# Kernel optimization log

Measured on AMD Instinct MI355X. Metric: run time of the kernel, lower is better.

## Reference

```python
import jax, jax.numpy as jnp
import numpy as np

B, D, K, H = 8192, 1024, 4096, 8


def setup_inputs() -> dict:
    key = jax.random.key(0)
    k1, k2 = jax.random.split(key)
    inputs = jax.random.normal(k1, (B, 1, D), dtype=jnp.float32)
    # Per-head codebooks; original init decays scale by init_decay_weight**hix,
    # emulate with a 0.5**h decay so later heads model smaller residuals.
    decay = (0.5 ** jnp.arange(H, dtype=jnp.float32)).reshape(H, 1, 1)
    codebooks = jax.random.normal(k2, (H, K, D), dtype=jnp.float32) * decay
    return {"inputs": inputs, "codebooks": codebooks}


def reference(inputs, codebooks):
    """Hierarchical refinement quantizer, eval path (hard argmin selection).

    Cascade over heads: distances to codebook -> argmin -> gather embedding
    -> subtract from residual -> next head. Returns (quantized_sum, codes).
    """
    x = inputs[:, 0, :]                      # [B, D]
    resid = x
    quantized = jnp.zeros_like(x)
    codes = []
    n_heads = codebooks.shape[0]
    for h in range(n_heads):                 # fixed, small head count
        E = codebooks[h]                     # [K, D]
        # squared euclidean distances: ||r||^2 - 2 r.E^T + ||E||^2  -> [B, K]
        dist = (
            jnp.sum(resid * resid, axis=-1, keepdims=True)
            - 2.0 * jnp.einsum("bd,kd->bk", resid, E)
            + jnp.sum(E * E, axis=-1)
        )
        idx = jnp.argmin(dist, axis=-1)      # [B]
        onehot = jax.nn.one_hot(idx, E.shape[0], dtype=resid.dtype)  # [B, K]
        q = onehot @ E                       # [B, D] gathered embedding
        quantized = quantized + q
        resid = resid - q
        codes.append(idx)
    vq_codes = jnp.stack(codes, axis=1)      # [B, H]
    return quantized, vq_codes
```

## Files before the change

kernel.cpp:

```cpp
#include <hip/hip_runtime.h>

#define B_ 8192
#define D_ 1024
#define K_ 4096
#define H_ 8

#define BM 128
#define BN 128
#define BK 32
#define NBLK 64
#define NCAND 6

typedef __attribute__((ext_vector_type(8))) short short8v;
typedef __attribute__((ext_vector_type(4))) float f32x4;

#define FINF 3.4e38f
#define IBIG 0x7fffffff

__device__ __forceinline__ void amin(float& v, int& i, float v2, int i2) {
    if (v2 < v || (v2 == v && i2 < i)) { v = v2; i = i2; }
}

__device__ __forceinline__ unsigned short f2bf_rn(float x) {
    unsigned int u = __float_as_uint(x);
    unsigned int r = (u + 0x7fffu + ((u >> 16) & 1u)) >> 16;
    return (unsigned short)r;
}

__device__ __forceinline__ void gload16(const unsigned short* g, unsigned short* l) {
    __builtin_amdgcn_global_load_lds(
        (const __attribute__((address_space(1))) void*)g,
        (__attribute__((address_space(3))) void*)l, 16, 0, 0);
}

__global__ __launch_bounds__(256) void cbconv_kernel(const float* __restrict__ E,
                                                     unsigned short* __restrict__ hi,
                                                     float* __restrict__ eeh) {
    const int row = blockIdx.x;
    const int t = threadIdx.x;
    float4 v = reinterpret_cast<const float4*>(E + (size_t)row * D_)[t];
    ushort4 h;
    h.x = f2bf_rn(v.x); h.y = f2bf_rn(v.y);
    h.z = f2bf_rn(v.z); h.w = f2bf_rn(v.w);
    reinterpret_cast<ushort4*>(hi + (size_t)row * D_)[t] = h;
    float s = v.x * v.x + v.y * v.y + v.z * v.z + v.w * v.w;
    #pragma unroll
    for (int m = 1; m < 64; m <<= 1) s += __shfl_xor(s, m);
    __shared__ float ls[4];
    if ((t & 63) == 0) ls[t >> 6] = s;
    __syncthreads();
    if (t == 0) eeh[row] = (ls[0] + ls[1]) + (ls[2] + ls[3]);
}

__global__ __launch_bounds__(256) void init_kernel(const float* __restrict__ x,
                                                   float* __restrict__ resid,
                                                   float* __restrict__ rr,
                                                   unsigned short* __restrict__ rhi) {
    const int b = blockIdx.x;
    const int t = threadIdx.x;
    float4 v = reinterpret_cast<const float4*>(x + (size_t)b * D_)[t];
    reinterpret_cast<float4*>(resid + (size_t)b * D_)[t] = v;
    ushort4 h;
    h.x = f2bf_rn(v.x); h.y = f2bf_rn(v.y);
    h.z = f2bf_rn(v.z); h.w = f2bf_rn(v.w);
    reinterpret_cast<ushort4*>(rhi + (size_t)b * D_)[t] = h;
    float s = v.x * v.x + v.y * v.y + v.z * v.z + v.w * v.w;
    #pragma unroll
    for (int m = 1; m < 64; m <<= 1) s += __shfl_xor(s, m);
    __shared__ float ls[4];
    if ((t & 63) == 0) ls[t >> 6] = s;
    __syncthreads();
    if (t == 0) rr[b] = (ls[0] + ls[1]) + (ls[2] + ls[3]);
}

__global__ __launch_bounds__(256) void score_mfma_kernel(
    const unsigned short* __restrict__ Ch,
    const unsigned short* __restrict__ Rh,
    const float* __restrict__ ee,
    float* __restrict__ pval, int* __restrict__ pidx) {
    __shared__ unsigned short lds[2][128][BK];

    const int tid = threadIdx.x;
    const int be0 = blockIdx.x * BN;
    const int br0 = blockIdx.y * BM;

    f32x4 acc[4][4];
    #pragma unroll
    for (int i = 0; i < 4; ++i)
        #pragma unroll
        for (int j = 0; j < 4; ++j)
            #pragma unroll
            for (int r = 0; r < 4; ++r) acc[i][j][r] = 0.f;

    const int srow = tid >> 2;
    const int sch  = (tid & 3) * 8;
    const size_t rstep = (size_t)64 * D_;
    const unsigned short* pC = Ch + (size_t)(be0 + srow) * D_ + sch;
    const unsigned short* pR = Rh + (size_t)(br0 + srow) * D_ + sch;

    const int l  = tid & 63;
    const int w  = tid >> 6;
    const int wr = (w >> 1) * 64;
    const int wc = (w & 1) * 64;
    const int fr = l & 15;
    const int k8 = (l >> 4) * 8;

    for (int d0 = 0; d0 < D_; d0 += BK) {
        __syncthreads();
        gload16(pC + d0,         &lds[0][srow][sch]);
        gload16(pC + rstep + d0, &lds[0][srow + 64][sch]);
        gload16(pR + d0,         &lds[1][srow][sch]);
        gload16(pR + rstep + d0, &lds[1][srow + 64][sch]);
        __syncthreads();

        short8v a_h[4], b_h[4];
        #pragma unroll
        for (int f = 0; f < 4; ++f) {
            a_h[f] = *reinterpret_cast<const short8v*>(&lds[0][wr + f * 16 + fr][k8]);
            b_h[f] = *reinterpret_cast<const short8v*>(&lds[1][wc + f * 16 + fr][k8]);
        }
        #pragma unroll
        for (int i = 0; i < 4; ++i)
            #pragma unroll
            for (int j = 0; j < 4; ++j)
                acc[i][j] = __builtin_amdgcn_mfma_f32_16x16x32_bf16(a_h[i], b_h[j], acc[i][j], 0, 0, 0);
    }

    const int g4 = (l >> 4) * 4;
    float eb[4][4];
    int ec[4][4];
    #pragma unroll
    for (int i = 0; i < 4; ++i)
        #pragma unroll
        for (int r = 0; r < 4; ++r) {
            ec[i][r] = be0 + wr + i * 16 + g4 + r;
            eb[i][r] = ee[ec[i][r]];
        }
    const int eblk = blockIdx.x * 2 + (w >> 1);

    #pragma unroll
    for (int j = 0; j < 4; ++j) {
        const int rrow = br0 + wc + j * 16 + fr;
        float b1 = FINF; int i1 = IBIG;
        float b2 = FINF; int i2 = IBIG;
        #pragma unroll
        for (int i = 0; i < 4; ++i)
            #pragma unroll
            for (int r = 0; r < 4; ++r) {
                const float s = fmaf(-2.0f, acc[i][j][r], eb[i][r]);
                const int c = ec[i][r];
                const bool lt = (s < b1) || (s == b1 && c < i1);
                const float lv = lt ? b1 : s;
                const int   li = lt ? i1 : c;
                if (lt) { b1 = s; i1 = c; }
                amin(b2, i2, lv, li);
            }
        #pragma unroll
        for (int m = 16; m < 64; m <<= 1) {
            const float o1 = __shfl_xor(b1, m); const int oi1 = __shfl_xor(i1, m);
            const float o2 = __shfl_xor(b2, m); const int oi2 = __shfl_xor(i2, m);
            const bool lt = (o1 < b1) || (o1 == b1 && oi1 < i1);
            const float lv = lt ? b1 : o1;
            const int   li = lt ? i1 : oi1;
            if (lt) { b1 = o1; i1 = oi1; }
            amin(b2, i2, o2, oi2);
            amin(b2, i2, lv, li);
        }
        if ((l >> 4) == 0) {
            const size_t base = ((size_t)rrow * NBLK + eblk) * 2;
            pval[base] = b1;     pidx[base] = i1;
            pval[base + 1] = b2; pidx[base + 1] = i2;
        }
    }
}

__global__ __launch_bounds__(256) void update_kernel(
    float* __restrict__ resid,
    const float* __restrict__ E,
    const float* __restrict__ ee,
    const float* __restrict__ pval,
    const int* __restrict__ pidx,
    float* __restrict__ rr,
    float* __restrict__ codes,
    unsigned short* __restrict__ rhi,
    const float* __restrict__ x,
    float* __restrict__ quant,
    int h) {
    const int w = threadIdx.x >> 6;
    const int l = threadIdx.x & 63;
    const int b = blockIdx.x * 4 + w;

    const size_t pbase = ((size_t)b * NBLK + l) * 2;
    float v0 = pval[pbase], v1 = pval[pbase + 1];
    int i0 = pidx[pbase], i1 = pidx[pbase + 1];
    int cand[NCAND];
    #pragma unroll
    for (int r = 0; r < NCAND; ++r) {
        float av = v0; int ai = i0;
        amin(av, ai, v1, i1);
        #pragma unroll
        for (int m = 1; m < 64; m <<= 1) {
            float ov = __shfl_xor(av, m);
            int oi = __shfl_xor(ai, m);
            amin(av, ai, ov, oi);
        }
        if (ai == i0) v0 = FINF;
        if (ai == i1) v1 = FINF;
        cand[r] = ai;
    }

    const float4* r4row = reinterpret_cast<const float4*>(resid + (size_t)b * D_);
    float4 rx[4];
    #pragma unroll
    for (int q = 0; q < 4; ++q) rx[q] = r4row[q * 64 + l];

    float dots[NCAND];
    #pragma unroll
    for (int c = 0; c < NCAND; ++c) {
        const float4* e4 = reinterpret_cast<const float4*>(E + (size_t)cand[c] * D_);
        float dot = 0.f;
        #pragma unroll
        for (int q = 0; q < 4; ++q) {
            float4 e = e4[q * 64 + l];
            dot = fmaf(rx[q].x, e.x, dot);
            dot = fmaf(rx[q].y, e.y, dot);
            dot = fmaf(rx[q].z, e.z, dot);
            dot = fmaf(rx[q].w, e.w, dot);
        }
        #pragma unroll
        for (int m = 1; m < 64; m <<= 1) dot += __shfl_xor(dot, m);
        dots[c] = dot;
    }

    const float rv = rr[b];
    float bv = FINF; int bi = IBIG;
    #pragma unroll
    for (int c = 0; c < NCAND; ++c) {
        const float s = (rv - 2.0f * dots[c]) + ee[cand[c]];
        amin(bv, bi, s, cand[c]);
    }
    if (l == 0) codes[(size_t)b * H_ + h] = (float)bi;

    const float4* q4 = reinterpret_cast<const float4*>(E + (size_t)bi * D_);
    float4* r4w = reinterpret_cast<float4*>(resid + (size_t)b * D_);
    ushort4* h4w = reinterpret_cast<ushort4*>(rhi + (size_t)b * D_);
    float nrm = 0.f;
    #pragma unroll
    for (int q = 0; q < 4; ++q) {
        float4 qv = q4[q * 64 + l];
        float4 r = rx[q];
        r.x -= qv.x; r.y -= qv.y; r.z -= qv.z; r.w -= qv.w;
        rx[q] = r;
        r4w[q * 64 + l] = r;
        ushort4 hh;
        hh.x = f2bf_rn(r.x); hh.y = f2bf_rn(r.y);
        hh.z = f2bf_rn(r.z); hh.w = f2bf_rn(r.w);
        h4w[q * 64 + l] = hh;
        nrm += r.x * r.x + r.y * r.y + r.z * r.z + r.w * r.w;
    }
    #pragma unroll
    for (int m = 1; m < 64; m <<= 1) nrm += __shfl_xor(nrm, m);
    if (l == 0) rr[b] = nrm;

    if (h == H_ - 1) {
        const float4* x4 = reinterpret_cast<const float4*>(x + (size_t)b * D_);
        float4* o4 = reinterpret_cast<float4*>(quant + (size_t)b * D_);
        #pragma unroll
        for (int q = 0; q < 4; ++q) {
            float4 xv = x4[q * 64 + l];
            float4 o;
            o.x = xv.x - rx[q].x; o.y = xv.y - rx[q].y;
            o.z = xv.z - rx[q].z; o.w = xv.w - rx[q].w;
            o4[q * 64 + l] = o;
        }
    }
}

extern "C" void kernel_launch(void* const* d_in, const int* in_sizes, int n_in,
                              void* d_out, int out_size, void* d_ws, size_t ws_size,
                              hipStream_t stream) {
    const float* x  = (const float*)d_in[0];
    const float* cb = (const float*)d_in[1];
    float* out = (float*)d_out;
    float* quant = out;
    float* codes = out + (size_t)B_ * D_;

    char* ws = (char*)d_ws;
    size_t off = 0;
    float* resid = (float*)(ws + off); off += (size_t)B_ * D_ * 4;
    float* rr    = (float*)(ws + off); off += (size_t)B_ * 4;
    float* ee    = (float*)(ws + off); off += (size_t)H_ * K_ * 4;
    float* pval  = (float*)(ws + off); off += (size_t)B_ * NBLK * 2 * 4;
    int*   pidx  = (int*)  (ws + off); off += (size_t)B_ * NBLK * 2 * 4;
    unsigned short* rhi = (unsigned short*)(ws + off); off += (size_t)B_ * D_ * 2;
    unsigned short* chi = (unsigned short*)(ws + off); off += (size_t)K_ * D_ * 2;

    hipLaunchKernelGGL(init_kernel, dim3(B_), dim3(256), 0, stream, x, resid, rr, rhi);

    for (int h = 0; h < H_; ++h) {
        const float* E  = cb + (size_t)h * K_ * D_;
        float* eh = ee + (size_t)h * K_;
        hipLaunchKernelGGL(cbconv_kernel, dim3(K_), dim3(256), 0, stream, E, chi, eh);
        hipLaunchKernelGGL(score_mfma_kernel, dim3(K_ / BN, B_ / BM), dim3(256), 0, stream,
                           chi, rhi, eh, pval, pidx);
        hipLaunchKernelGGL(update_kernel, dim3(B_ / 4), dim3(256), 0, stream,
                           resid, E, eh, pval, pidx, rr, codes, rhi, x, quant, h);
    }
}
```

Before: 1.183 ms.

## Rewrite score GEMM as 256x256 tile with double-buffered swizzled LDS pipeline

The bf16 MFMA scoring kernel moves from 128x128 tiles with a single LDS buffer and two barriers per BK=32 step to 256x256 tiles with 512 threads, BK=64, double-buffered dynamic LDS (128KB) and an XOR-swizzled layout. Global loads for the next k-tile are issued in stages interleaved with MFMA phases, with explicit waitcnt, barriers and setprio. This targets better data reuse, overlap of loads with compute, and fewer LDS bank conflicts. Because each wave now covers 128 codebook entries, the kernel keeps a top-3 per block instead of top-2 to preserve candidate quality, and the update kernel reads 32 blocks times 3 candidates. The risks are higher register pressure from 8x4 accumulators, the large LDS footprint limiting occupancy, and relying on hand-tuned wait counts being correct.

```diff
diff --git a/kernel.cpp b/kernel.cpp
--- a/kernel.cpp
+++ b/kernel.cpp
@@ -5,10 +5,8 @@
 #define K_ 4096
 #define H_ 8
 
-#define BM 128
-#define BN 128
-#define BK 32
-#define NBLK 64
+#define NBLK 32
+#define TOPB 3
 #define NCAND 6
 
 typedef __attribute__((ext_vector_type(8))) short short8v;
@@ -73,105 +71,174 @@
     if (t == 0) rr[b] = (ls[0] + ls[1]) + (ls[2] + ls[3]);
 }
 
-__global__ __launch_bounds__(256) void score_mfma_kernel(
+__global__ __launch_bounds__(512, 2) void score_mfma_kernel(
     const unsigned short* __restrict__ Ch,
     const unsigned short* __restrict__ Rh,
     const float* __restrict__ ee,
     float* __restrict__ pval, int* __restrict__ pidx) {
-    __shared__ unsigned short lds[2][128][BK];
+    extern __shared__ unsigned short lds_dyn[];
 
     const int tid = threadIdx.x;
-    const int be0 = blockIdx.x * BN;
-    const int br0 = blockIdx.y * BM;
-
-    f32x4 acc[4][4];
-    #pragma unroll
-    for (int i = 0; i < 4; ++i)
+    const int l = tid & 63;
+    const int w = tid >> 6;
+    const int wE = w >> 2;
+    const int wR = w & 3;
+    const int be0 = blockIdx.x * 256;
+    const int br0 = blockIdx.y * 256;
+
+    f32x4 acc[8][4];
+    #pragma unroll
+    for (int i = 0; i < 8; ++i)
         #pragma unroll
         for (int j = 0; j < 4; ++j)
             #pragma unroll
             for (int r = 0; r < 4; ++r) acc[i][j][r] = 0.f;
 
-    const int srow = tid >> 2;
-    const int sch  = (tid & 3) * 8;
-    const size_t rstep = (size_t)64 * D_;
-    const unsigned short* pC = Ch + (size_t)(be0 + srow) * D_ + sch;
-    const unsigned short* pR = Rh + (size_t)(br0 + srow) * D_ + sch;
-
-    const int l  = tid & 63;
-    const int w  = tid >> 6;
-    const int wr = (w >> 1) * 64;
-    const int wc = (w & 1) * 64;
+    const int row0 = (w << 4) + (l >> 3);
+    const int lch  = (l & 7) ^ ((l >> 3) & 7);
+    const int dst0 = (w << 10) + (l << 3);
+    const unsigned short* gsrc0 = Ch + (size_t)(be0 +       row0) * D_ + lch * 8;
+    const unsigned short* gsrc1 = Ch + (size_t)(be0 + 128 + row0) * D_ + lch * 8;
+    const unsigned short* gsrc2 = Rh + (size_t)(br0 +       row0) * D_ + lch * 8;
+    const unsigned short* gsrc3 = Rh + (size_t)(br0 + 128 + row0) * D_ + lch * 8;
+
+    #define STAGE(kt_, ht_) do {                                                  \
+        unsigned short* _d = lds_dyn + ((((((kt_) & 1) << 2) + (ht_))) << 13) + dst0; \
+        const unsigned short* _g = gsrc##ht_ + ((size_t)(kt_) << 6);              \
+        gload16(_g, _d);                                                          \
+        gload16(_g + (size_t)8 * D_, _d + 512);                                   \
+    } while (0)
+
     const int fr = l & 15;
-    const int k8 = (l >> 4) * 8;
-
-    for (int d0 = 0; d0 < D_; d0 += BK) {
-        __syncthreads();
-        gload16(pC + d0,         &lds[0][srow][sch]);
-        gload16(pC + rstep + d0, &lds[0][srow + 64][sch]);
-        gload16(pR + d0,         &lds[1][srow][sch]);
-        gload16(pR + rstep + d0, &lds[1][srow + 64][sch]);
-        __syncthreads();
-
-        short8v a_h[4], b_h[4];
-        #pragma unroll
-        for (int f = 0; f < 4; ++f) {
-            a_h[f] = *reinterpret_cast<const short8v*>(&lds[0][wr + f * 16 + fr][k8]);
-            b_h[f] = *reinterpret_cast<const short8v*>(&lds[1][wc + f * 16 + fr][k8]);
-        }
-        #pragma unroll
-        for (int i = 0; i < 4; ++i)
+    const int lg = l >> 4;
+    const int f7 = l & 7;
+    const int ck0 = lg ^ f7;
+    const int ck1 = (4 | lg) ^ f7;
+
+    STAGE(0, 0); STAGE(0, 1); STAGE(0, 2); STAGE(0, 3);
+
+    for (int kt = 0; kt < 16; ++kt) {
+        const int p = kt & 1;
+        const unsigned short* LA = lds_dyn + (((p << 2) + wE) << 13) + fr * 64;
+        const unsigned short* LB = lds_dyn + (((p << 2) + 2 + (wR >> 1)) << 13)
+                                   + (((wR & 1) << 6) + fr) * 64;
+        short8v bf0[4], bf1[4], af0[2], af1[2];
+
+        if (kt < 15) {
+            STAGE(kt + 1, 0);
+            asm volatile("s_waitcnt vmcnt(2)" ::: "memory");
+        } else {
+            asm volatile("s_waitcnt vmcnt(0)" ::: "memory");
+        }
+        __builtin_amdgcn_sched_barrier(0);
+        __builtin_amdgcn_s_barrier();
+        __builtin_amdgcn_sched_barrier(0);
+        #pragma unroll
+        for (int j = 0; j < 4; ++j) {
+            bf0[j] = *reinterpret_cast<const short8v*>(LB + (j << 10) + (ck0 << 3));
+            bf1[j] = *reinterpret_cast<const short8v*>(LB + (j << 10) + (ck1 << 3));
+        }
+        af0[0] = *reinterpret_cast<const short8v*>(LA + (ck0 << 3));
+        af1[0] = *reinterpret_cast<const short8v*>(LA + (ck1 << 3));
+        af0[1] = *reinterpret_cast<const short8v*>(LA + (1 << 10) + (ck0 << 3));
+        af1[1] = *reinterpret_cast<const short8v*>(LA + (1 << 10) + (ck1 << 3));
+        asm volatile("s_waitcnt lgkmcnt(0)" ::: "memory");
+        __builtin_amdgcn_sched_barrier(0);
+        __builtin_amdgcn_s_setprio(1);
+        #pragma unroll
+        for (int ii = 0; ii < 2; ++ii)
             #pragma unroll
-            for (int j = 0; j < 4; ++j)
-                acc[i][j] = __builtin_amdgcn_mfma_f32_16x16x32_bf16(a_h[i], b_h[j], acc[i][j], 0, 0, 0);
-    }
-
-    const int g4 = (l >> 4) * 4;
-    float eb[4][4];
-    int ec[4][4];
-    #pragma unroll
-    for (int i = 0; i < 4; ++i)
+            for (int j = 0; j < 4; ++j) {
+                acc[ii][j] = __builtin_amdgcn_mfma_f32_16x16x32_bf16(af0[ii], bf0[j], acc[ii][j], 0, 0, 0);
+                acc[ii][j] = __builtin_amdgcn_mfma_f32_16x16x32_bf16(af1[ii], bf1[j], acc[ii][j], 0, 0, 0);
+            }
+        __builtin_amdgcn_s_setprio(0);
+        __builtin_amdgcn_sched_barrier(0);
+        __builtin_amdgcn_s_barrier();
+        __builtin_amdgcn_sched_barrier(0);
+
+        #pragma unroll
+        for (int q = 1; q < 4; ++q) {
+            af0[0] = *reinterpret_cast<const short8v*>(LA + ((2 * q) << 10) + (ck0 << 3));
+            af1[0] = *reinterpret_cast<const short8v*>(LA + ((2 * q) << 10) + (ck1 << 3));
+            af0[1] = *reinterpret_cast<const short8v*>(LA + ((2 * q + 1) << 10) + (ck0 << 3));
+            af1[1] = *reinterpret_cast<const short8v*>(LA + ((2 * q + 1) << 10) + (ck1 << 3));
+            if (kt < 15) {
+                if (q == 1) STAGE(kt + 1, 1);
+                else if (q == 2) STAGE(kt + 1, 2);
+                else STAGE(kt + 1, 3);
+            }
+            __builtin_amdgcn_sched_barrier(0);
+            __builtin_amdgcn_s_barrier();
+            __builtin_amdgcn_sched_barrier(0);
+            asm volatile("s_waitcnt lgkmcnt(0)" ::: "memory");
+            __builtin_amdgcn_sched_barrier(0);
+            __builtin_amdgcn_s_setprio(1);
+            #pragma unroll
+            for (int ii = 0; ii < 2; ++ii)
+                #pragma unroll
+                for (int j = 0; j < 4; ++j) {
+                    acc[2 * q + ii][j] = __builtin_amdgcn_mfma_f32_16x16x32_bf16(af0[ii], bf0[j], acc[2 * q + ii][j], 0, 0, 0);
+                    acc[2 * q + ii][j] = __builtin_amdgcn_mfma_f32_16x16x32_bf16(af1[ii], bf1[j], acc[2 * q + ii][j], 0, 0, 0);
+                }
+            __builtin_amdgcn_s_setprio(0);
+            __builtin_amdgcn_sched_barrier(0);
+            __builtin_amdgcn_s_barrier();
+            __builtin_amdgcn_sched_barrier(0);
+        }
+    }
+    #undef STAGE
+
+    const int g4 = lg << 2;
+    float ev[8][4];
+    int ecd[8][4];
+    #pragma unroll
+    for (int i = 0; i < 8; ++i)
         #pragma unroll
         for (int r = 0; r < 4; ++r) {
-            ec[i][r] = be0 + wr + i * 16 + g4 + r;
-            eb[i][r] = ee[ec[i][r]];
-        }
-    const int eblk = blockIdx.x * 2 + (w >> 1);
+            ecd[i][r] = be0 + wE * 128 + i * 16 + g4 + r;
+            ev[i][r] = ee[ecd[i][r]];
+        }
+    const int eblk = blockIdx.x * 2 + wE;
+
+    #define INS3(v, c) do {                                         \
+        const float _v = (v); const int _c = (c);                   \
+        if (_v < b1 || (_v == b1 && _c < i1)) {                     \
+            b3 = b2; i3 = i2; b2 = b1; i2 = i1; b1 = _v; i1 = _c;   \
+        } else if (_v < b2 || (_v == b2 && _c < i2)) {              \
+            b3 = b2; i3 = i2; b2 = _v; i2 = _c;                     \
+        } else if (_v < b3 || (_v == b3 && _c < i3)) {              \
+            b3 = _v; i3 = _c;                                       \
+        }                                                           \
+    } while (0)
 
     #pragma unroll
     for (int j = 0; j < 4; ++j) {
-        const int rrow = br0 + wc + j * 16 + fr;
-        float b1 = FINF; int i1 = IBIG;
-        float b2 = FINF; int i2 = IBIG;
-        #pragma unroll
-        for (int i = 0; i < 4; ++i)
+        const int rrow = br0 + wR * 64 + j * 16 + fr;
+        float b1 = FINF, b2 = FINF, b3 = FINF;
+        int i1 = IBIG, i2 = IBIG, i3 = IBIG;
+        #pragma unroll
+        for (int i = 0; i < 8; ++i)
             #pragma unroll
             for (int r = 0; r < 4; ++r) {
-                const float s = fmaf(-2.0f, acc[i][j][r], eb[i][r]);
-                const int c = ec[i][r];
-                const bool lt = (s < b1) || (s == b1 && c < i1);
-                const float lv = lt ? b1 : s;
-                const int   li = lt ? i1 : c;
-                if (lt) { b1 = s; i1 = c; }
-                amin(b2, i2, lv, li);
+                const float s = fmaf(-2.0f, acc[i][j][r], ev[i][r]);
+                INS3(s, ecd[i][r]);
             }
         #pragma unroll
         for (int m = 16; m < 64; m <<= 1) {
             const float o1 = __shfl_xor(b1, m); const int oi1 = __shfl_xor(i1, m);
             const float o2 = __shfl_xor(b2, m); const int oi2 = __shfl_xor(i2, m);
-            const bool lt = (o1 < b1) || (o1 == b1 && oi1 < i1);
-            const float lv = lt ? b1 : o1;
-            const int   li = lt ? i1 : oi1;
-            if (lt) { b1 = o1; i1 = oi1; }
-            amin(b2, i2, o2, oi2);
-            amin(b2, i2, lv, li);
-        }
-        if ((l >> 4) == 0) {
-            const size_t base = ((size_t)rrow * NBLK + eblk) * 2;
+            const float o3 = __shfl_xor(b3, m); const int oi3 = __shfl_xor(i3, m);
+            INS3(o1, oi1); INS3(o2, oi2); INS3(o3, oi3);
+        }
+        if (lg == 0) {
+            const size_t base = ((size_t)rrow * NBLK + eblk) * TOPB;
             pval[base] = b1;     pidx[base] = i1;
             pval[base + 1] = b2; pidx[base + 1] = i2;
-        }
-    }
+            pval[base + 2] = b3; pidx[base + 2] = i3;
+        }
+    }
+    #undef INS3
 }
 
 __global__ __launch_bounds__(256) void update_kernel(
@@ -190,14 +257,20 @@
     const int l = threadIdx.x & 63;
     const int b = blockIdx.x * 4 + w;
 
-    const size_t pbase = ((size_t)b * NBLK + l) * 2;
-    float v0 = pval[pbase], v1 = pval[pbase + 1];
-    int i0 = pidx[pbase], i1 = pidx[pbase + 1];
+    float v0 = FINF, v1 = FINF, v2 = FINF;
+    int i0 = IBIG, i1 = IBIG, i2 = IBIG;
+    if (l < NBLK) {
+        const size_t pbase = ((size_t)b * NBLK + l) * TOPB;
+        v0 = pval[pbase];     i0 = pidx[pbase];
+        v1 = pval[pbase + 1]; i1 = pidx[pbase + 1];
+        v2 = pval[pbase + 2]; i2 = pidx[pbase + 2];
+    }
     int cand[NCAND];
     #pragma unroll
     for (int r = 0; r < NCAND; ++r) {
         float av = v0; int ai = i0;
         amin(av, ai, v1, i1);
+        amin(av, ai, v2, i2);
         #pragma unroll
         for (int m = 1; m < 64; m <<= 1) {
             float ov = __shfl_xor(av, m);
@@ -206,6 +279,7 @@
         }
         if (ai == i0) v0 = FINF;
         if (ai == i1) v1 = FINF;
+        if (ai == i2) v2 = FINF;
         cand[r] = ai;
     }
 
@@ -290,8 +364,8 @@
     float* resid = (float*)(ws + off); off += (size_t)B_ * D_ * 4;
     float* rr    = (float*)(ws + off); off += (size_t)B_ * 4;
     float* ee    = (float*)(ws + off); off += (size_t)H_ * K_ * 4;
-    float* pval  = (float*)(ws + off); off += (size_t)B_ * NBLK * 2 * 4;
-    int*   pidx  = (int*)  (ws + off); off += (size_t)B_ * NBLK * 2 * 4;
+    float* pval  = (float*)(ws + off); off += (size_t)B_ * NBLK * TOPB * 4;
+    int*   pidx  = (int*)  (ws + off); off += (size_t)B_ * NBLK * TOPB * 4;
     unsigned short* rhi = (unsigned short*)(ws + off); off += (size_t)B_ * D_ * 2;
     unsigned short* chi = (unsigned short*)(ws + off); off += (size_t)K_ * D_ * 2;
 
@@ -301,8 +375,8 @@
         const float* E  = cb + (size_t)h * K_ * D_;
         float* eh = ee + (size_t)h * K_;
         hipLaunchKernelGGL(cbconv_kernel, dim3(K_), dim3(256), 0, stream, E, chi, eh);
-        hipLaunchKernelGGL(score_mfma_kernel, dim3(K_ / BN, B_ / BM), dim3(256), 0, stream,
-                           chi, rhi, eh, pval, pidx);
+        hipLaunchKernelGGL(score_mfma_kernel, dim3(K_ / 256, B_ / 256), dim3(512),
+                           131072, stream, chi, rhi, eh, pval, pidx);
         hipLaunchKernelGGL(update_kernel, dim3(B_ / 4), dim3(256), 0, stream,
                            resid, E, eh, pval, pidx, rr, codes, rhi, x, quant, h);
     }
```

After: 1.207 ms. +2.1%, slower.
